# Optimization experiments

Measured on AMD Instinct MI355X. Metric: run time of the kernel, lower is better.

Reference implementation:

```python
import jax, jax.numpy as jnp
import numpy as np

D_MODEL = 1024
D_CTRL = 1024
N_HEADS = 16
TOPK = 4
TEMPERATURE = 1.0
LN_EPS = 1e-5


def layer_norm(x, g, b):
    m = jnp.mean(x, axis=-1, keepdims=True)
    v = jnp.mean(jnp.square(x - m), axis=-1, keepdims=True)
    return (x - m) * jax.lax.rsqrt(v + LN_EPS) * g + b


def setup_inputs() -> dict:
    key = jax.random.key(0)
    ks = jax.random.split(key, 8)
    B, S = 8, 2048
    s = 0.02
    return {
        "x": jax.random.normal(ks[0], (B, S, D_MODEL), dtype=jnp.float32),
        "state": jnp.zeros((B, D_CTRL), dtype=jnp.float32),
        # pool LayerNorm
        "pool_g": jnp.ones((D_MODEL,), jnp.float32),
        "pool_b": jnp.zeros((D_MODEL,), jnp.float32),
        # inp_proj
        "inp_w": jax.random.normal(ks[1], (D_MODEL, D_CTRL), jnp.float32) * s,
        "inp_b": jnp.zeros((D_CTRL,), jnp.float32),
        # W_z, W_h
        "wz_w": jax.random.normal(ks[2], (D_CTRL, D_CTRL), jnp.float32) * s,
        "wz_b": jnp.zeros((D_CTRL,), jnp.float32),
        "wh_w": jax.random.normal(ks[3], (D_CTRL, D_CTRL), jnp.float32) * s,
        "wh_b": jnp.zeros((D_CTRL,), jnp.float32),
        # ln_h
        "lnh_g": jnp.ones((D_CTRL,), jnp.float32),
        "lnh_b": jnp.zeros((D_CTRL,), jnp.float32),
        # router: LayerNorm(d_model+d_ctrl) -> Linear -> GELU -> Linear
        "rln_g": jnp.ones((D_MODEL + D_CTRL,), jnp.float32),
        "rln_b": jnp.zeros((D_MODEL + D_CTRL,), jnp.float32),
        "r_w1": jax.random.normal(ks[4], (D_MODEL + D_CTRL, D_CTRL), jnp.float32) * s,
        "r_b1": jnp.zeros((D_CTRL,), jnp.float32),
        "r_w2": jax.random.normal(ks[5], (D_CTRL, N_HEADS), jnp.float32) * s,
        "r_b2": jnp.zeros((N_HEADS,), jnp.float32),
    }


def reference(x, state, pool_g, pool_b, inp_w, inp_b, wz_w, wz_b, wh_w, wh_b,
              lnh_g, lnh_b, rln_g, rln_b, r_w1, r_b1, r_w2, r_b2):
    B, S, D = x.shape
    # pool: LayerNorm over tokens then mean over sequence -> [B, d_model]
    g = jnp.mean(layer_norm(x, pool_g, pool_b), axis=1)
    x_ctrl = g @ inp_w + inp_b  # [B, d_ctrl]
    z = jax.nn.sigmoid(x_ctrl @ wz_w + wz_b)
    h_cand = jnp.tanh(x_ctrl @ wh_w + wh_b)
    h_new = (1.0 - z) * state + z * h_cand
    h_new = layer_norm(h_new, lnh_g, lnh_b)  # [B, d_ctrl]
    # token-conditioned router on concat([X, h_tok])
    h_tok = jnp.broadcast_to(h_new[:, None, :], (B, S, D_CTRL))
    cat = jnp.concatenate([x, h_tok], axis=-1)  # [B, S, d_model+d_ctrl]
    hid = jax.nn.gelu(layer_norm(cat, rln_g, rln_b) @ r_w1 + r_b1, approximate=False)
    logits = hid @ r_w2 + r_b2  # [B, S, H]
    alpha = jax.nn.softmax(logits / TEMPERATURE, axis=-1)
    # top-k mask + renorm
    _, topi = jax.lax.top_k(alpha, TOPK)  # [B, S, k]
    mask = jnp.sum(jax.nn.one_hot(topi, N_HEADS, dtype=alpha.dtype), axis=-2)  # [B, S, H]
    masked = alpha * mask
    denom = jnp.maximum(jnp.sum(masked, axis=-1, keepdims=True), 1e-12)
    alpha = masked / denom
    entropy = -jnp.mean(jnp.sum(alpha * jnp.log(jnp.maximum(alpha, 1e-12)), axis=-1))
    return (alpha, h_new, entropy)
```

## Files before the change

kernel.cpp:

```cpp
#include <hip/hip_runtime.h>
#include <hip/hip_bf16.h>
#include <math.h>

typedef unsigned short u16;
typedef __attribute__((ext_vector_type(8))) short bf16x8;
typedef __attribute__((ext_vector_type(4))) float f32x4;
typedef __attribute__((ext_vector_type(4))) unsigned short u16x4;

#define B_ 8
#define S_ 2048
#define T_ 16384
#define D_ 1024
#define H_ 16
#define EPS_ 1e-5f

__device__ __forceinline__ u16 f2bf(float f) {
    __hip_bfloat16 h = __float2bfloat16(f);
    union { __hip_bfloat16 h; u16 u; } cv; cv.h = h; return cv.u;
}
__device__ __forceinline__ float bf2f(u16 u) {
    union { u16 u; __hip_bfloat16 h; } cv; cv.u = u; return __bfloat162float(cv.h);
}

__global__ __launch_bounds__(256) void k0a(const float* __restrict__ rw1,
        const float* __restrict__ rlng, const float* __restrict__ rlnb,
        u16* __restrict__ whiT, u16* __restrict__ wloT,
        float* __restrict__ c1part, float* __restrict__ c2part) {
    int nb = blockIdx.x, kb = blockIdx.y;
    int t = threadIdx.x;
    int nl = t & 63, kq = t >> 6;
    int n0 = nb * 64, k0 = kb * 64;
    __shared__ float ld[64][65];
    __shared__ float red[2][4][64];
    float a1 = 0.f, a2 = 0.f;
    #pragma unroll
    for (int r = 0; r < 16; ++r) {
        int kl = r * 4 + kq;
        int k = k0 + kl, n = n0 + nl;
        float w0 = rw1[(size_t)k * 1024 + n];
        ld[kl][nl] = w0;
        a1 += rlng[k] * w0;
        a2 += rlnb[k] * w0;
    }
    red[0][kq][nl] = a1;
    red[1][kq][nl] = a2;
    __syncthreads();
    if (t < 64) {
        c1part[(size_t)kb * 1024 + n0 + t] = red[0][0][t] + red[0][1][t] + red[0][2][t] + red[0][3][t];
        c2part[(size_t)kb * 1024 + n0 + t] = red[1][0][t] + red[1][1][t] + red[1][2][t] + red[1][3][t];
    }
    if (kb < 16) {
        #pragma unroll
        for (int r = 0; r < 16; ++r) {
            int nl2 = r * 4 + kq;
            int k = k0 + nl, n = n0 + nl2;
            float w0 = ld[nl][nl2] * rlng[k];
            u16 hi = f2bf(w0);
            float lo = w0 - bf2f(hi);
            whiT[(size_t)n * 1024 + k] = hi;
            wloT[(size_t)n * 1024 + k] = f2bf(lo);
        }
    }
}

__global__ __launch_bounds__(256) void k0b(const float* __restrict__ c1part,
        const float* __restrict__ c2part, const float* __restrict__ rb1,
        float* __restrict__ c1, float* __restrict__ dvec) {
    int n = blockIdx.x * 256 + threadIdx.x;
    float s1 = 0.f, s2 = 0.f;
    for (int p = 0; p < 32; ++p) { s1 += c1part[p * 1024 + n]; s2 += c2part[p * 1024 + n]; }
    c1[n] = s1;
    dvec[n] = s2 + rb1[n];
}

__global__ __launch_bounds__(256) void k1(const float* __restrict__ x,
        u16* __restrict__ xhi, u16* __restrict__ xlo,
        float* __restrict__ sx, float* __restrict__ sxx, float* __restrict__ gpart) {
    int blk = blockIdx.x;
    int b = blk >> 5, chunk = blk & 31;
    int tid = threadIdx.x, w = tid >> 6, lane = tid & 63;
    __shared__ float lacc[4][1024];
    float acc[4][4];
    #pragma unroll
    for (int j = 0; j < 4; ++j)
        #pragma unroll
        for (int c = 0; c < 4; ++c) acc[j][c] = 0.f;

    for (int i = 0; i < 16; ++i) {
        int s = chunk * 64 + i * 4 + w;
        size_t tok = (size_t)b * S_ + s;
        size_t base = tok * D_;
        float4 v[4];
        float sum = 0.f, ssq = 0.f;
        #pragma unroll
        for (int j = 0; j < 4; ++j) {
            v[j] = *(const float4*)&x[base + j * 256 + lane * 4];
            sum += v[j].x + v[j].y + v[j].z + v[j].w;
            ssq += v[j].x * v[j].x + v[j].y * v[j].y + v[j].z * v[j].z + v[j].w * v[j].w;
        }
        #pragma unroll
        for (int m = 1; m < 64; m <<= 1) { sum += __shfl_xor(sum, m); ssq += __shfl_xor(ssq, m); }
        float mean = sum * (1.f / 1024.f);
        float var = ssq * (1.f / 1024.f) - mean * mean;
        float rstd = rsqrtf(var + EPS_);
        if (lane == 0) { sx[tok] = sum; sxx[tok] = ssq; }
        #pragma unroll
        for (int j = 0; j < 4; ++j) {
            float xs[4] = { v[j].x, v[j].y, v[j].z, v[j].w };
            u16 hs[4], ls[4];
            #pragma unroll
            for (int c = 0; c < 4; ++c) {
                acc[j][c] += (xs[c] - mean) * rstd;
                u16 h = f2bf(xs[c]);
                hs[c] = h;
                ls[c] = f2bf(xs[c] - bf2f(h));
            }
            size_t o = base + j * 256 + lane * 4;
            *(u16x4*)&xhi[o] = (u16x4){ hs[0], hs[1], hs[2], hs[3] };
            *(u16x4*)&xlo[o] = (u16x4){ ls[0], ls[1], ls[2], ls[3] };
        }
    }
    #pragma unroll
    for (int j = 0; j < 4; ++j)
        #pragma unroll
        for (int c = 0; c < 4; ++c) lacc[w][j * 256 + lane * 4 + c] = acc[j][c];
    __syncthreads();
    for (int q = 0; q < 4; ++q) {
        int n = q * 256 + tid;
        gpart[((size_t)b * 32 + chunk) * 1024 + n] =
            lacc[0][n] + lacc[1][n] + lacc[2][n] + lacc[3][n];
    }
}

__global__ __launch_bounds__(256) void k2(const float* __restrict__ gpart,
        const float* __restrict__ pg, const float* __restrict__ pb, float* __restrict__ g) {
    int i = blockIdx.x * 256 + threadIdx.x;
    int b = i >> 10, n = i & 1023;
    float s = 0.f;
    for (int p = 0; p < 32; ++p) s += gpart[((size_t)b * 32 + p) * 1024 + n];
    g[i] = s * (1.f / 2048.f) * pg[n] + pb[n];
}

__global__ __launch_bounds__(256) void kgemv_split(const float* __restrict__ in,
        const float* __restrict__ W, const float* __restrict__ scale,
        float* __restrict__ part) {
    int t = threadIdx.x;
    int n = blockIdx.x * 256 + t;
    int k0 = blockIdx.y * 32;
    __shared__ float sg[8][32];
    {
        int b = t >> 5, k = t & 31;
        float v = in[b * 1024 + k0 + k];
        if (scale) v *= scale[k0 + k];
        sg[b][k] = v;
    }
    __syncthreads();
    float acc[8] = {};
    #pragma unroll
    for (int k = 0; k < 32; ++k) {
        float wv = W[(size_t)(k0 + k) * 1024 + n];
        #pragma unroll
        for (int b = 0; b < 8; ++b) acc[b] += sg[b][k] * wv;
    }
    #pragma unroll
    for (int b = 0; b < 8; ++b)
        part[((size_t)blockIdx.y * 8 + b) * 1024 + n] = acc[b];
}

__global__ __launch_bounds__(256) void kgemv2_split(const float* __restrict__ in,
        const float* __restrict__ Wz, const float* __restrict__ Wh,
        float* __restrict__ zpart, float* __restrict__ hpart) {
    int t = threadIdx.x;
    int n = blockIdx.x * 256 + t;
    int k0 = blockIdx.y * 32;
    __shared__ float sg[8][32];
    {
        int b = t >> 5, k = t & 31;
        sg[b][k] = in[b * 1024 + k0 + k];
    }
    __syncthreads();
    float az[8] = {}, ah[8] = {};
    #pragma unroll
    for (int k = 0; k < 32; ++k) {
        size_t o = (size_t)(k0 + k) * 1024 + n;
        float wz = Wz[o];
        float wh = Wh[o];
        #pragma unroll
        for (int b = 0; b < 8; ++b) { az[b] += sg[b][k] * wz; ah[b] += sg[b][k] * wh; }
    }
    #pragma unroll
    for (int b = 0; b < 8; ++b) {
        size_t o = ((size_t)blockIdx.y * 8 + b) * 1024 + n;
        zpart[o] = az[b];
        hpart[o] = ah[b];
    }
}

__global__ __launch_bounds__(256) void kred_bias(const float* __restrict__ part,
        const float* __restrict__ bias, float* __restrict__ out) {
    int i = blockIdx.x * 256 + threadIdx.x;
    int b = i >> 10, n = i & 1023;
    float s = bias ? bias[n] : 0.f;
    #pragma unroll 8
    for (int p = 0; p < 32; ++p) s += part[((size_t)p * 8 + b) * 1024 + n];
    out[i] = s;
}

__global__ __launch_bounds__(256) void k3b_red_ln(const float* __restrict__ zpart,
        const float* __restrict__ hpart, const float* __restrict__ bz,
        const float* __restrict__ bh, const float* __restrict__ state,
        const float* __restrict__ lg, const float* __restrict__ lb,
        float* __restrict__ hnew, float* __restrict__ outh,
        float* __restrict__ shb, float* __restrict__ shhb) {
    int b = blockIdx.x, tid = threadIdx.x;
    int w = tid >> 6, lane = tid & 63;
    __shared__ float rbuf[4][2];
    float hp[4];
    float sum = 0.f, ssq = 0.f;
    #pragma unroll
    for (int q = 0; q < 4; ++q) {
        int n = q * 256 + tid;
        float az = bz[n], ah = bh[n];
        #pragma unroll 8
        for (int p = 0; p < 32; ++p) {
            size_t o = ((size_t)p * 8 + b) * 1024 + n;
            az += zpart[o];
            ah += hpart[o];
        }
        float z = 1.f / (1.f + expf(-az));
        float hc = tanhf(ah);
        float v = (1.f - z) * state[(size_t)b * 1024 + n] + z * hc;
        hp[q] = v; sum += v; ssq += v * v;
    }
    #pragma unroll
    for (int m = 1; m < 64; m <<= 1) { sum += __shfl_xor(sum, m); ssq += __shfl_xor(ssq, m); }
    if (lane == 0) { rbuf[w][0] = sum; rbuf[w][1] = ssq; }
    __syncthreads();
    sum = rbuf[0][0] + rbuf[1][0] + rbuf[2][0] + rbuf[3][0];
    ssq = rbuf[0][1] + rbuf[1][1] + rbuf[2][1] + rbuf[3][1];
    float mean = sum * (1.f / 1024.f);
    float var = ssq * (1.f / 1024.f) - mean * mean;
    float rstd = rsqrtf(var + EPS_);
    float s2 = 0.f, q2 = 0.f;
    #pragma unroll
    for (int q = 0; q < 4; ++q) {
        int n = q * 256 + tid;
        float h = (hp[q] - mean) * rstd * lg[n] + lb[n];
        hnew[(size_t)b * 1024 + n] = h;
        outh[(size_t)b * 1024 + n] = h;
        s2 += h; q2 += h * h;
    }
    #pragma unroll
    for (int m = 1; m < 64; m <<= 1) { s2 += __shfl_xor(s2, m); q2 += __shfl_xor(q2, m); }
    __syncthreads();
    if (lane == 0) { rbuf[w][0] = s2; rbuf[w][1] = q2; }
    __syncthreads();
    if (tid == 0) {
        shb[b] = rbuf[0][0] + rbuf[1][0] + rbuf[2][0] + rbuf[3][0];
        shhb[b] = rbuf[0][1] + rbuf[1][1] + rbuf[2][1] + rbuf[3][1];
    }
}

__global__ __launch_bounds__(256) void k4b(const float* __restrict__ sx,
        const float* __restrict__ sxx, const float* __restrict__ shb,
        const float* __restrict__ shhb, float* __restrict__ pt, float* __restrict__ qt) {
    int t = blockIdx.x * 256 + threadIdx.x;
    int b = t >> 11;
    float m = (sx[t] + shb[b]) * (1.f / 2048.f);
    float var = (sxx[t] + shhb[b]) * (1.f / 2048.f) - m * m;
    float rstd = rsqrtf(var + EPS_);
    pt[t] = rstd;
    qt[t] = -m * rstd;
}

__device__ __forceinline__ void gl16(const void* g, void* l) {
    __builtin_amdgcn_global_load_lds((const __attribute__((address_space(1))) void*)g,
                                     (__attribute__((address_space(3))) void*)l, 16, 0, 0);
}

__global__ __launch_bounds__(256, 1) void k5_gemm(
        const u16* __restrict__ xhi, const u16* __restrict__ xlo,
        const u16* __restrict__ whiT, const u16* __restrict__ wloT,
        const float* __restrict__ pt, const float* __restrict__ qt,
        const float* __restrict__ vmat, const float* __restrict__ c1,
        const float* __restrict__ dvec, const float* __restrict__ rw2,
        float* __restrict__ lpart) {
    __shared__ unsigned char smem[66048];
    u16* sAh = (u16*)smem;
    u16* sAl = sAh + 128 * 64;
    u16* sBh = sAl + 128 * 64;
    u16* sBl = sBh + 128 * 64;
    float* shid = (float*)smem;

    int nb = blockIdx.x, mb = blockIdx.y;
    int tid = threadIdx.x;
    int lane = tid & 63, wid = tid >> 6;
    int wm = wid >> 1, wn = wid & 1;
    int l16 = lane & 15, lq = lane >> 4;

    f32x4 acc[4][4] = {};

    size_t aBase = (size_t)mb * 128 * 1024;
    size_t bBase = (size_t)nb * 128 * 1024;

    for (int kb = 0; kb < 16; ++kb) {
        __syncthreads();
        #pragma unroll
        for (int i = 0; i < 4; ++i) {
            int chunk = tid + 256 * i;
            int row = chunk >> 3, c8 = chunk & 7;
            size_t go = (size_t)row * 1024 + (size_t)kb * 64 + c8 * 8;
            int lo = chunk * 16;
            gl16(xhi + aBase + go, (char*)sAh + lo);
            gl16(xlo + aBase + go, (char*)sAl + lo);
            gl16(whiT + bBase + go, (char*)sBh + lo);
            gl16(wloT + bBase + go, (char*)sBl + lo);
        }
        asm volatile("s_waitcnt vmcnt(0)" ::: "memory");
        __syncthreads();
        #pragma unroll
        for (int kk = 0; kk < 2; ++kk) {
            bf16x8 ah[4], al[4], bh[4], bl[4];
            int ko = kk * 32 + lq * 8;
            #pragma unroll
            for (int f = 0; f < 4; ++f) {
                int ar = wm * 64 + f * 16 + l16;
                int br = wn * 64 + f * 16 + l16;
                ah[f] = *(const bf16x8*)&sAh[ar * 64 + ko];
                al[f] = *(const bf16x8*)&sAl[ar * 64 + ko];
                bh[f] = *(const bf16x8*)&sBh[br * 64 + ko];
                bl[f] = *(const bf16x8*)&sBl[br * 64 + ko];
            }
            #pragma unroll
            for (int mf = 0; mf < 4; ++mf)
                #pragma unroll
                for (int nf = 0; nf < 4; ++nf) {
                    acc[mf][nf] = __builtin_amdgcn_mfma_f32_16x16x32_bf16(ah[mf], bh[nf], acc[mf][nf], 0, 0, 0);
                    acc[mf][nf] = __builtin_amdgcn_mfma_f32_16x16x32_bf16(ah[mf], bl[nf], acc[mf][nf], 0, 0, 0);
                    acc[mf][nf] = __builtin_amdgcn_mfma_f32_16x16x32_bf16(al[mf], bh[nf], acc[mf][nf], 0, 0, 0);
                }
        }
    }
    __syncthreads();

    int token0 = mb * 128;
    int bidx = token0 >> 11;
    const float* vrow = vmat + (size_t)bidx * 1024;
    float vn[4], c1n[4], dn[4];
    #pragma unroll
    for (int nf = 0; nf < 4; ++nf) {
        int n = nb * 128 + wn * 64 + nf * 16 + l16;
        vn[nf] = vrow[n]; c1n[nf] = c1[n]; dn[nf] = dvec[n];
    }
    #pragma unroll
    for (int mf = 0; mf < 4; ++mf) {
        #pragma unroll
        for (int r = 0; r < 4; ++r) {
            int rowl = wm * 64 + mf * 16 + lq * 4 + r;
            float p = pt[token0 + rowl];
            float q = qt[token0 + rowl];
            #pragma unroll
            for (int nf = 0; nf < 4; ++nf) {
                int coll = wn * 64 + nf * 16 + l16;
                float pre = p * (acc[mf][nf][r] + vn[nf]) + q * c1n[nf] + dn[nf];
                float hid = 0.5f * pre * (1.f + erff(pre * 0.70710678118f));
                shid[rowl * 129 + coll] = hid;
            }
        }
    }
    __syncthreads();

    int r2 = tid >> 1, half = tid & 1;
    const float* w2b = rw2 + (size_t)nb * 128 * 16 + half * 8;
    float a8[8];
    #pragma unroll
    for (int h = 0; h < 8; ++h) a8[h] = 0.f;
    #pragma unroll 8
    for (int j = 0; j < 128; ++j) {
        float hv = shid[r2 * 129 + j];
        float4 w0 = *(const float4*)(w2b + (size_t)j * 16);
        float4 w1 = *(const float4*)(w2b + (size_t)j * 16 + 4);
        a8[0] += hv * w0.x; a8[1] += hv * w0.y; a8[2] += hv * w0.z; a8[3] += hv * w0.w;
        a8[4] += hv * w1.x; a8[5] += hv * w1.y; a8[6] += hv * w1.z; a8[7] += hv * w1.w;
    }
    float* lp = lpart + ((size_t)nb * T_ + token0 + r2) * 16 + half * 8;
    #pragma unroll
    for (int h = 0; h < 8; ++h) lp[h] = a8[h];
}

__global__ __launch_bounds__(256) void k6(const float* __restrict__ lpart,
        const float* __restrict__ rb2, float* __restrict__ alpha_out,
        float* __restrict__ entpart) {
    int blk = blockIdx.x;
    int tid = threadIdx.x;
    int token = blk * 16 + (tid >> 4);
    int h = tid & 15;
    float lg = rb2[h];
    #pragma unroll
    for (int p = 0; p < 8; ++p) lg += lpart[((size_t)p * T_ + token) * 16 + h];

    float mx = lg;
    #pragma unroll
    for (int m = 1; m < 16; m <<= 1) mx = fmaxf(mx, __shfl_xor(mx, m));
    float e = expf(lg - mx);
    float sum = e;
    #pragma unroll
    for (int m = 1; m < 16; m <<= 1) sum += __shfl_xor(sum, m);
    float a0 = e / sum;

    float work = lg;
    bool sel = false;
    #pragma unroll
    for (int it = 0; it < 4; ++it) {
        float bv = work; int bi = h;
        #pragma unroll
        for (int m = 1; m < 16; m <<= 1) {
            float ov = __shfl_xor(bv, m); int oi = __shfl_xor(bi, m);
            if (ov > bv || (ov == bv && oi < bi)) { bv = ov; bi = oi; }
        }
        if (h == bi) { sel = true; work = -1e30f; }
    }
    float am = sel ? a0 : 0.f;
    float den = am;
    #pragma unroll
    for (int m = 1; m < 16; m <<= 1) den += __shfl_xor(den, m);
    den = fmaxf(den, 1e-12f);
    float a = am / den;
    alpha_out[(size_t)token * 16 + h] = a;

    float term = a * logf(fmaxf(a, 1e-12f));
    #pragma unroll
    for (int m = 1; m < 64; m <<= 1) term += __shfl_xor(term, m);
    __shared__ float tw[4];
    if ((tid & 63) == 0) tw[tid >> 6] = term;
    __syncthreads();
    if (tid == 0) entpart[blk] = tw[0] + tw[1] + tw[2] + tw[3];
}

__global__ __launch_bounds__(256) void k7(const float* __restrict__ entpart,
        float* __restrict__ out_ent) {
    int tid = threadIdx.x;
    float s = 0.f;
    for (int i = tid; i < 1024; i += 256) s += entpart[i];
    #pragma unroll
    for (int m = 1; m < 64; m <<= 1) s += __shfl_xor(s, m);
    __shared__ float tw[4];
    if ((tid & 63) == 0) tw[tid >> 6] = s;
    __syncthreads();
    if (tid == 0) out_ent[0] = -(tw[0] + tw[1] + tw[2] + tw[3]) * (1.f / (float)T_);
}

extern "C" void kernel_launch(void* const* d_in, const int* in_sizes, int n_in,
                              void* d_out, int out_size, void* d_ws, size_t ws_size,
                              hipStream_t stream) {
    const float* x     = (const float*)d_in[0];
    const float* state = (const float*)d_in[1];
    const float* pg    = (const float*)d_in[2];
    const float* pbv   = (const float*)d_in[3];
    const float* inpw  = (const float*)d_in[4];
    const float* inpb  = (const float*)d_in[5];
    const float* wzw   = (const float*)d_in[6];
    const float* wzb   = (const float*)d_in[7];
    const float* whw   = (const float*)d_in[8];
    const float* whb   = (const float*)d_in[9];
    const float* lnhg  = (const float*)d_in[10];
    const float* lnhb  = (const float*)d_in[11];
    const float* rlng  = (const float*)d_in[12];
    const float* rlnb  = (const float*)d_in[13];
    const float* rw1   = (const float*)d_in[14];
    const float* rb1   = (const float*)d_in[15];
    const float* rw2   = (const float*)d_in[16];
    const float* rb2   = (const float*)d_in[17];
    float* out = (float*)d_out;
    (void)in_sizes; (void)n_in; (void)out_size; (void)ws_size;

    char* base = (char*)d_ws;
    size_t off = 0;
    auto alloc = [&](size_t bytes) -> char* {
        char* p = base + off;
        off = (off + bytes + 255) & ~(size_t)255;
        return p;
    };
    u16*   xhi    = (u16*)alloc((size_t)T_ * D_ * 2);
    u16*   xlo    = (u16*)alloc((size_t)T_ * D_ * 2);
    u16*   whiT   = (u16*)alloc((size_t)D_ * D_ * 2);
    u16*   wloT   = (u16*)alloc((size_t)D_ * D_ * 2);
    float* c1part = (float*)alloc(32 * 1024 * 4);
    float* c2part = (float*)alloc(32 * 1024 * 4);
    float* c1     = (float*)alloc(1024 * 4);
    float* dvec   = (float*)alloc(1024 * 4);
    float* sx     = (float*)alloc((size_t)T_ * 4);
    float* sxx    = (float*)alloc((size_t)T_ * 4);
    float* ptv    = (float*)alloc((size_t)T_ * 4);
    float* qtv    = (float*)alloc((size_t)T_ * 4);
    float* gpart  = (float*)alloc((size_t)8 * 32 * 1024 * 4);
    float* gvec   = (float*)alloc(8 * 1024 * 4);
    float* xctrl  = (float*)alloc(8 * 1024 * 4);
    float* hnew   = (float*)alloc(8 * 1024 * 4);
    float* shb    = (float*)alloc(256);
    float* shhb   = (float*)alloc(256);
    float* vmat   = (float*)alloc(8 * 1024 * 4);
    float* lpart  = (float*)alloc((size_t)8 * T_ * H_ * 4);
    float* entpart= (float*)alloc(1024 * 4);
    float* partA  = (float*)alloc((size_t)32 * 8 * 1024 * 4);
    float* partB  = (float*)alloc((size_t)32 * 8 * 1024 * 4);

    k0a<<<dim3(16, 32), 256, 0, stream>>>(rw1, rlng, rlnb, whiT, wloT, c1part, c2part);
    k0b<<<4, 256, 0, stream>>>(c1part, c2part, rb1, c1, dvec);
    k1<<<256, 256, 0, stream>>>(x, xhi, xlo, sx, sxx, gpart);
    k2<<<32, 256, 0, stream>>>(gpart, pg, pbv, gvec);
    kgemv_split<<<dim3(4, 32), 256, 0, stream>>>(gvec, inpw, nullptr, partA);
    kred_bias<<<32, 256, 0, stream>>>(partA, inpb, xctrl);
    kgemv2_split<<<dim3(4, 32), 256, 0, stream>>>(xctrl, wzw, whw, partA, partB);
    k3b_red_ln<<<8, 256, 0, stream>>>(partA, partB, wzb, whb, state, lnhg, lnhb,
                                      hnew, out + (size_t)T_ * H_, shb, shhb);
    kgemv_split<<<dim3(4, 32), 256, 0, stream>>>(hnew, rw1 + (size_t)1024 * 1024,
                                                 rlng + 1024, partA);
    kred_bias<<<32, 256, 0, stream>>>(partA, nullptr, vmat);
    k4b<<<64, 256, 0, stream>>>(sx, sxx, shb, shhb, ptv, qtv);
    k5_gemm<<<dim3(8, 128), 256, 0, stream>>>(xhi, xlo, whiT, wloT, ptv, qtv, vmat, c1, dvec, rw2, lpart);
    k6<<<1024, 256, 0, stream>>>(lpart, rb2, out, entpart);
    k7<<<1, 256, 0, stream>>>(entpart, out + (size_t)T_ * H_ + (size_t)B_ * D_);
}
```

Before: 241.1 us.

## Fuse small reduction kernels into consumers and double-buffer the GEMM K loop

Removes five small kernels (k0b, k2, kred_bias twice, k4b) by folding their partial-sum reductions and per-token LayerNorm stat computation into the kernels that consume them, which cuts launch count and intermediate round-trips. The main MFMA GEMM now uses a 32-wide K step with two LDS stages, prefetching the next tile while computing the current one, instead of a load-wait-compute loop with a full vmcnt(0) drain. Consumers now redundantly re-reduce 32 partials per block, which adds some duplicated global reads in the GEMM epilogue and the gemv prologues. The smaller K step also doubles the number of loop iterations and barriers.

```diff
diff --git a/kernel.cpp b/kernel.cpp
--- a/kernel.cpp
+++ b/kernel.cpp
@@ -61,16 +61,6 @@
             wloT[(size_t)n * 1024 + k] = f2bf(lo);
         }
     }
-}
-
-__global__ __launch_bounds__(256) void k0b(const float* __restrict__ c1part,
-        const float* __restrict__ c2part, const float* __restrict__ rb1,
-        float* __restrict__ c1, float* __restrict__ dvec) {
-    int n = blockIdx.x * 256 + threadIdx.x;
-    float s1 = 0.f, s2 = 0.f;
-    for (int p = 0; p < 32; ++p) { s1 += c1part[p * 1024 + n]; s2 += c2part[p * 1024 + n]; }
-    c1[n] = s1;
-    dvec[n] = s2 + rb1[n];
 }
 
 __global__ __launch_bounds__(256) void k1(const float* __restrict__ x,
@@ -132,13 +122,31 @@
     }
 }
 
-__global__ __launch_bounds__(256) void k2(const float* __restrict__ gpart,
-        const float* __restrict__ pg, const float* __restrict__ pb, float* __restrict__ g) {
-    int i = blockIdx.x * 256 + threadIdx.x;
-    int b = i >> 10, n = i & 1023;
-    float s = 0.f;
-    for (int p = 0; p < 32; ++p) s += gpart[((size_t)b * 32 + p) * 1024 + n];
-    g[i] = s * (1.f / 2048.f) * pg[n] + pb[n];
+__global__ __launch_bounds__(256) void kgemv_g(const float* __restrict__ gpart,
+        const float* __restrict__ pg, const float* __restrict__ pb,
+        const float* __restrict__ W, float* __restrict__ part) {
+    int t = threadIdx.x;
+    int n = blockIdx.x * 256 + t;
+    int k0 = blockIdx.y * 32;
+    __shared__ float sg[8][32];
+    {
+        int b = t >> 5, k = t & 31;
+        float s = 0.f;
+        #pragma unroll 8
+        for (int p = 0; p < 32; ++p) s += gpart[((size_t)b * 32 + p) * 1024 + k0 + k];
+        sg[b][k] = s * (1.f / 2048.f) * pg[k0 + k] + pb[k0 + k];
+    }
+    __syncthreads();
+    float acc[8] = {};
+    #pragma unroll
+    for (int k = 0; k < 32; ++k) {
+        float wv = W[(size_t)(k0 + k) * 1024 + n];
+        #pragma unroll
+        for (int b = 0; b < 8; ++b) acc[b] += sg[b][k] * wv;
+    }
+    #pragma unroll
+    for (int b = 0; b < 8; ++b)
+        part[((size_t)blockIdx.y * 8 + b) * 1024 + n] = acc[b];
 }
 
 __global__ __launch_bounds__(256) void kgemv_split(const float* __restrict__ in,
@@ -167,7 +175,8 @@
         part[((size_t)blockIdx.y * 8 + b) * 1024 + n] = acc[b];
 }
 
-__global__ __launch_bounds__(256) void kgemv2_split(const float* __restrict__ in,
+__global__ __launch_bounds__(256) void kgemv2_f(const float* __restrict__ partIn,
+        const float* __restrict__ bias,
         const float* __restrict__ Wz, const float* __restrict__ Wh,
         float* __restrict__ zpart, float* __restrict__ hpart) {
     int t = threadIdx.x;
@@ -176,7 +185,10 @@
     __shared__ float sg[8][32];
     {
         int b = t >> 5, k = t & 31;
-        sg[b][k] = in[b * 1024 + k0 + k];
+        float s = bias[k0 + k];
+        #pragma unroll 8
+        for (int p = 0; p < 32; ++p) s += partIn[((size_t)p * 8 + b) * 1024 + k0 + k];
+        sg[b][k] = s;
     }
     __syncthreads();
     float az[8] = {}, ah[8] = {};
@@ -194,16 +206,6 @@
         zpart[o] = az[b];
         hpart[o] = ah[b];
     }
-}
-
-__global__ __launch_bounds__(256) void kred_bias(const float* __restrict__ part,
-        const float* __restrict__ bias, float* __restrict__ out) {
-    int i = blockIdx.x * 256 + threadIdx.x;
-    int b = i >> 10, n = i & 1023;
-    float s = bias ? bias[n] : 0.f;
-    #pragma unroll 8
-    for (int p = 0; p < 32; ++p) s += part[((size_t)p * 8 + b) * 1024 + n];
-    out[i] = s;
 }
 
 __global__ __launch_bounds__(256) void k3b_red_ln(const float* __restrict__ zpart,
@@ -261,18 +263,6 @@
     }
 }
 
-__global__ __launch_bounds__(256) void k4b(const float* __restrict__ sx,
-        const float* __restrict__ sxx, const float* __restrict__ shb,
-        const float* __restrict__ shhb, float* __restrict__ pt, float* __restrict__ qt) {
-    int t = blockIdx.x * 256 + threadIdx.x;
-    int b = t >> 11;
-    float m = (sx[t] + shb[b]) * (1.f / 2048.f);
-    float var = (sxx[t] + shhb[b]) * (1.f / 2048.f) - m * m;
-    float rstd = rsqrtf(var + EPS_);
-    pt[t] = rstd;
-    qt[t] = -m * rstd;
-}
-
 __device__ __forceinline__ void gl16(const void* g, void* l) {
     __builtin_amdgcn_global_load_lds((const __attribute__((address_space(1))) void*)g,
                                      (__attribute__((address_space(3))) void*)l, 16, 0, 0);
@@ -281,15 +271,12 @@
 __global__ __launch_bounds__(256, 1) void k5_gemm(
         const u16* __restrict__ xhi, const u16* __restrict__ xlo,
         const u16* __restrict__ whiT, const u16* __restrict__ wloT,
-        const float* __restrict__ pt, const float* __restrict__ qt,
-        const float* __restrict__ vmat, const float* __restrict__ c1,
-        const float* __restrict__ dvec, const float* __restrict__ rw2,
-        float* __restrict__ lpart) {
+        const float* __restrict__ sx, const float* __restrict__ sxx,
+        const float* __restrict__ shb, const float* __restrict__ shhb,
+        const float* __restrict__ vpart, const float* __restrict__ c1part,
+        const float* __restrict__ c2part, const float* __restrict__ rb1,
+        const float* __restrict__ rw2, float* __restrict__ lpart) {
     __shared__ unsigned char smem[66048];
-    u16* sAh = (u16*)smem;
-    u16* sAl = sAh + 128 * 64;
-    u16* sBh = sAl + 128 * 64;
-    u16* sBl = sBh + 128 * 64;
     float* shid = (float*)smem;
 
     int nb = blockIdx.x, mb = blockIdx.y;
@@ -299,66 +286,81 @@
     int l16 = lane & 15, lq = lane >> 4;
 
     f32x4 acc[4][4] = {};
-
     size_t aBase = (size_t)mb * 128 * 1024;
     size_t bBase = (size_t)nb * 128 * 1024;
 
-    for (int kb = 0; kb < 16; ++kb) {
+    auto STAGE = [&](int kb, int s) {
+        unsigned char* st = smem + s * 32768;
+        #pragma unroll
+        for (int i = 0; i < 2; ++i) {
+            int chunk = tid + 256 * i;
+            int row = chunk >> 2, c4 = chunk & 3;
+            size_t go = (size_t)row * 1024 + (size_t)kb * 32 + c4 * 8;
+            int lo = chunk * 16;
+            gl16(xhi + aBase + go, st + lo);
+            gl16(xlo + aBase + go, st + 8192 + lo);
+            gl16(whiT + bBase + go, st + 16384 + lo);
+            gl16(wloT + bBase + go, st + 24576 + lo);
+        }
+    };
+
+    STAGE(0, 0);
+    __syncthreads();
+
+    int buf = 0;
+    for (int kb = 0; kb < 32; ++kb) {
+        if (kb < 31) STAGE(kb + 1, buf ^ 1);
+        const u16* sAh = (const u16*)(smem + buf * 32768);
+        const u16* sAl = sAh + 4096;
+        const u16* sBh = sAl + 4096;
+        const u16* sBl = sBh + 4096;
+        bf16x8 ah[4], al[4], bh[4], bl[4];
+        #pragma unroll
+        for (int f = 0; f < 4; ++f) {
+            int ar = wm * 64 + f * 16 + l16;
+            int br = wn * 64 + f * 16 + l16;
+            ah[f] = *(const bf16x8*)&sAh[ar * 32 + lq * 8];
+            al[f] = *(const bf16x8*)&sAl[ar * 32 + lq * 8];
+            bh[f] = *(const bf16x8*)&sBh[br * 32 + lq * 8];
+            bl[f] = *(const bf16x8*)&sBl[br * 32 + lq * 8];
+        }
+        #pragma unroll
+        for (int mf = 0; mf < 4; ++mf)
+            #pragma unroll
+            for (int nf = 0; nf < 4; ++nf) {
+                acc[mf][nf] = __builtin_amdgcn_mfma_f32_16x16x32_bf16(ah[mf], bh[nf], acc[mf][nf], 0, 0, 0);
+                acc[mf][nf] = __builtin_amdgcn_mfma_f32_16x16x32_bf16(ah[mf], bl[nf], acc[mf][nf], 0, 0, 0);
+                acc[mf][nf] = __builtin_amdgcn_mfma_f32_16x16x32_bf16(al[mf], bh[nf], acc[mf][nf], 0, 0, 0);
+            }
         __syncthreads();
-        #pragma unroll
-        for (int i = 0; i < 4; ++i) {
-            int chunk = tid + 256 * i;
-            int row = chunk >> 3, c8 = chunk & 7;
-            size_t go = (size_t)row * 1024 + (size_t)kb * 64 + c8 * 8;
-            int lo = chunk * 16;
-            gl16(xhi + aBase + go, (char*)sAh + lo);
-            gl16(xlo + aBase + go, (char*)sAl + lo);
-            gl16(whiT + bBase + go, (char*)sBh + lo);
-            gl16(wloT + bBase + go, (char*)sBl + lo);
-        }
-        asm volatile("s_waitcnt vmcnt(0)" ::: "memory");
-        __syncthreads();
-        #pragma unroll
-        for (int kk = 0; kk < 2; ++kk) {
-            bf16x8 ah[4], al[4], bh[4], bl[4];
-            int ko = kk * 32 + lq * 8;
-            #pragma unroll
-            for (int f = 0; f < 4; ++f) {
-                int ar = wm * 64 + f * 16 + l16;
-                int br = wn * 64 + f * 16 + l16;
-                ah[f] = *(const bf16x8*)&sAh[ar * 64 + ko];
-                al[f] = *(const bf16x8*)&sAl[ar * 64 + ko];
-                bh[f] = *(const bf16x8*)&sBh[br * 64 + ko];
-                bl[f] = *(const bf16x8*)&sBl[br * 64 + ko];
-            }
-            #pragma unroll
-            for (int mf = 0; mf < 4; ++mf)
-                #pragma unroll
-                for (int nf = 0; nf < 4; ++nf) {
-                    acc[mf][nf] = __builtin_amdgcn_mfma_f32_16x16x32_bf16(ah[mf], bh[nf], acc[mf][nf], 0, 0, 0);
-                    acc[mf][nf] = __builtin_amdgcn_mfma_f32_16x16x32_bf16(ah[mf], bl[nf], acc[mf][nf], 0, 0, 0);
-                    acc[mf][nf] = __builtin_amdgcn_mfma_f32_16x16x32_bf16(al[mf], bh[nf], acc[mf][nf], 0, 0, 0);
-                }
-        }
-    }
-    __syncthreads();
+        buf ^= 1;
+    }
 
     int token0 = mb * 128;
     int bidx = token0 >> 11;
-    const float* vrow = vmat + (size_t)bidx * 1024;
     float vn[4], c1n[4], dn[4];
     #pragma unroll
     for (int nf = 0; nf < 4; ++nf) {
         int n = nb * 128 + wn * 64 + nf * 16 + l16;
-        vn[nf] = vrow[n]; c1n[nf] = c1[n]; dn[nf] = dvec[n];
-    }
+        float sv = 0.f, s1 = 0.f, s2 = 0.f;
+        for (int p = 0; p < 32; ++p) {
+            sv += vpart[((size_t)p * 8 + bidx) * 1024 + n];
+            s1 += c1part[(size_t)p * 1024 + n];
+            s2 += c2part[(size_t)p * 1024 + n];
+        }
+        vn[nf] = sv; c1n[nf] = s1; dn[nf] = s2 + rb1[n];
+    }
+    float sH = shb[bidx], sHH = shhb[bidx];
     #pragma unroll
     for (int mf = 0; mf < 4; ++mf) {
         #pragma unroll
         for (int r = 0; r < 4; ++r) {
             int rowl = wm * 64 + mf * 16 + lq * 4 + r;
-            float p = pt[token0 + rowl];
-            float q = qt[token0 + rowl];
+            int tok = token0 + rowl;
+            float m = (sx[tok] + sH) * (1.f / 2048.f);
+            float var = (sxx[tok] + sHH) * (1.f / 2048.f) - m * m;
+            float p = rsqrtf(var + EPS_);
+            float q = -m * p;
             #pragma unroll
             for (int nf = 0; nf < 4; ++nf) {
                 int coll = wn * 64 + nf * 16 + l16;
@@ -487,38 +489,28 @@
     u16*   wloT   = (u16*)alloc((size_t)D_ * D_ * 2);
     float* c1part = (float*)alloc(32 * 1024 * 4);
     float* c2part = (float*)alloc(32 * 1024 * 4);
-    float* c1     = (float*)alloc(1024 * 4);
-    float* dvec   = (float*)alloc(1024 * 4);
     float* sx     = (float*)alloc((size_t)T_ * 4);
     float* sxx    = (float*)alloc((size_t)T_ * 4);
-    float* ptv    = (float*)alloc((size_t)T_ * 4);
-    float* qtv    = (float*)alloc((size_t)T_ * 4);
     float* gpart  = (float*)alloc((size_t)8 * 32 * 1024 * 4);
-    float* gvec   = (float*)alloc(8 * 1024 * 4);
-    float* xctrl  = (float*)alloc(8 * 1024 * 4);
     float* hnew   = (float*)alloc(8 * 1024 * 4);
     float* shb    = (float*)alloc(256);
     float* shhb   = (float*)alloc(256);
-    float* vmat   = (float*)alloc(8 * 1024 * 4);
     float* lpart  = (float*)alloc((size_t)8 * T_ * H_ * 4);
     float* entpart= (float*)alloc(1024 * 4);
     float* partA  = (float*)alloc((size_t)32 * 8 * 1024 * 4);
     float* partB  = (float*)alloc((size_t)32 * 8 * 1024 * 4);
+    float* partC  = (float*)alloc((size_t)32 * 8 * 1024 * 4);
 
     k0a<<<dim3(16, 32), 256, 0, stream>>>(rw1, rlng, rlnb, whiT, wloT, c1part, c2part);
-    k0b<<<4, 256, 0, stream>>>(c1part, c2part, rb1, c1, dvec);
     k1<<<256, 256, 0, stream>>>(x, xhi, xlo, sx, sxx, gpart);
-    k2<<<32, 256, 0, stream>>>(gpart, pg, pbv, gvec);
-    kgemv_split<<<dim3(4, 32), 256, 0, stream>>>(gvec, inpw, nullptr, partA);
-    kred_bias<<<32, 256, 0, stream>>>(partA, inpb, xctrl);
-    kgemv2_split<<<dim3(4, 32), 256, 0, stream>>>(xctrl, wzw, whw, partA, partB);
-    k3b_red_ln<<<8, 256, 0, stream>>>(partA, partB, wzb, whb, state, lnhg, lnhb,
+    kgemv_g<<<dim3(4, 32), 256, 0, stream>>>(gpart, pg, pbv, inpw, partA);
+    kgemv2_f<<<dim3(4, 32), 256, 0, stream>>>(partA, inpb, wzw, whw, partB, partC);
+    k3b_red_ln<<<8, 256, 0, stream>>>(partB, partC, wzb, whb, state, lnhg, lnhb,
                                       hnew, out + (size_t)T_ * H_, shb, shhb);
     kgemv_split<<<dim3(4, 32), 256, 0, stream>>>(hnew, rw1 + (size_t)1024 * 1024,
                                                  rlng + 1024, partA);
-    kred_bias<<<32, 256, 0, stream>>>(partA, nullptr, vmat);
-    k4b<<<64, 256, 0, stream>>>(sx, sxx, shb, shhb, ptv, qtv);
-    k5_gemm<<<dim3(8, 128), 256, 0, stream>>>(xhi, xlo, whiT, wloT, ptv, qtv, vmat, c1, dvec, rw2, lpart);
+    k5_gemm<<<dim3(8, 128), 256, 0, stream>>>(xhi, xlo, whiT, wloT, sx, sxx, shb, shhb,
+                                              partA, c1part, c2part, rb1, rw2, lpart);
     k6<<<1024, 256, 0, stream>>>(lpart, rb2, out, entpart);
     k7<<<1, 256, 0, stream>>>(entpart, out + (size_t)T_ * H_ + (size_t)B_ * D_);
 }
```

Measured after the change: 302.9 us. 25.7% more time.
